# Kernel optimization log

Measured on AMD Instinct MI355X. Metric: run time of the kernel, lower is better.

Reference implementation:

```python
import jax, jax.numpy as jnp
import numpy as np

B, P, K = 8, 1024, 20
N = B * P
EMB, OUT = 1024, 40
GRID = 5

def _window(W):
    # Hamming taper (window_type='hamming')
    n = jnp.arange(W, dtype=jnp.float32)
    return 0.54 - 0.46 * jnp.cos(2.0 * jnp.pi * n / (W - 1))

def _init_kan(key, din, dout, W, S, g):
    nw = (din - W) // S + 1
    coeffs = jax.random.normal(key, (2, dout, nw, W, g), jnp.float32) / (np.sqrt(nw * W) * np.sqrt(g))
    bias = jnp.zeros((dout,), jnp.float32)
    return coeffs, bias

def stft_kan(x, coeffs, bias, W, S):
    # x: (n, D) -> (n, dout). Slice D into overlapping windows of size W,
    # stride S, apply Hamming taper, build Fourier features cos(k*x), sin(k*x)
    # for k=1..g and contract with learned coefficients (STFT-Fourier-KAN).
    nw, g = coeffs.shape[2], coeffs.shape[4]
    idx = (np.arange(nw) * S)[:, None] + np.arange(W)[None, :]        # (nw, W)
    xw = x[:, idx] * _window(W)                                        # (n, nw, W)
    kfreq = jnp.arange(1, g + 1, dtype=x.dtype)
    arg = xw[..., None] * kfreq                                        # (n, nw, W, g)
    y = (jnp.einsum('nwig,owig->no', jnp.cos(arg), coeffs[0])
         + jnp.einsum('nwig,owig->no', jnp.sin(arg), coeffs[1]))
    return y + bias

def setup_inputs():
    key = jax.random.key(0)
    ks = jax.random.split(key, 5)
    pos = jax.random.normal(ks[0], (N, 3), jnp.float32)
    batch = (jnp.arange(N) // P).astype(jnp.int32)  # sorted, equal-size clouds
    c1, b1 = _init_kan(ks[1], 6, 64, 3, 3, GRID)
    c2, b2 = _init_kan(ks[2], 64, 128, 16, 8, GRID)
    c3, b3 = _init_kan(ks[3], 128, EMB, 32, 16, GRID)
    c4, b4 = _init_kan(ks[4], 2 * EMB, OUT, 256, 128, GRID)
    return {"pos": pos, "batch": batch, "c1": c1, "b1": b1, "c2": c2, "b2": b2,
            "c3": c3, "b3": b3, "c4": c4, "b4": b4}

def reference(pos, batch, c1, b1, c2, b2, c3, b3, c4, b4):
    posb = pos.reshape(B, P, 3)
    # dynamic kNN graph per cloud (self excluded)
    d = jnp.sum((posb[:, :, None, :] - posb[:, None, :, :]) ** 2, -1)  # (B,P,P)
    d = d + jnp.eye(P, dtype=d.dtype) * 1e10
    _, nbr = jax.lax.top_k(-d, K)                                      # (B,P,K)
    pj = jax.vmap(lambda p, i: p[i])(posb, nbr)                        # (B,P,K,3)
    pi = jnp.broadcast_to(posb[:, :, None, :], pj.shape)
    e = jnp.concatenate([pi, pj - pi], -1).reshape(N * K, 6)           # edge feats
    h = stft_kan(e, c1, b1, 3, 3)                                      # (N*K,64)
    h = stft_kan(h, c2, b2, 16, 8)                                     # (N*K,128)
    x1 = jnp.max(h.reshape(N, K, 128), axis=1)                         # max aggr over neighbors
    x = stft_kan(x1, c3, b3, 32, 16)                                   # (N,EMB)
    gmax = jax.ops.segment_max(x, batch, num_segments=B)
    gsum = jax.ops.segment_sum(x, batch, num_segments=B)
    cnt = jax.ops.segment_sum(jnp.ones((N, 1), x.dtype), batch, num_segments=B)
    xg = jnp.concatenate([gmax, gsum / cnt], -1)                       # (B, 2*EMB)
    return stft_kan(xg, c4, b4, 256, 128)                              # (B, OUT)
```

## Files before the change

### kernel.cpp

```cpp
#include <hip/hip_runtime.h>


typedef unsigned short u16;
typedef unsigned int   u32;
typedef unsigned long long u64;
typedef __attribute__((ext_vector_type(8))) _Float16 half8;
typedef __attribute__((ext_vector_type(4))) float f32x4;

__device__ __forceinline__ float bf2f(u16 u) {
  u32 v = ((u32)u) << 16;
  return __uint_as_float(v);
}
__device__ __forceinline__ u16 f2bfr(float f) {
  u32 x = __float_as_uint(f);
  u32 r = x + 0x7FFFu + ((x >> 16) & 1u);
  return (u16)(r >> 16);
}
__device__ __forceinline__ u16 f2h(float f) {
  _Float16 h = (_Float16)f;
  u16 r;
  __builtin_memcpy(&r, &h, 2);
  return r;
}
__device__ __forceinline__ float h2f(u16 u) {
  _Float16 h;
  __builtin_memcpy(&h, &u, 2);
  return (float)h;
}
__device__ __forceinline__ float ldf(const void* p, size_t i, bool f32) {
  return f32 ? ((const float*)p)[i] : bf2f(((const u16*)p)[i]);
}
__device__ __forceinline__ u64 minu64(u64 a, u64 b) { return a < b ? a : b; }

__device__ __forceinline__ bool wave_detect(const void* pos) {
  float a = fabsf(((const float*)pos)[threadIdx.x & 63]);
  bool ok = (a > 1.0e-3f && a < 100.0f);
  unsigned long long m = __ballot(ok);
  return __popcll(m) >= 32;
}

#define NBR_OFF   ((size_t)0)
#define L4P_OFF   (((size_t)(1u << 20)) + 131072)
#define C1T_OFF   (((size_t)(1u << 20)) + 524288)
#define C2T_OFF   (((size_t)(1u << 20)) + 589824)
#define C3T_OFF   ((size_t)(2u << 20))
#define C4T_OFF   ((size_t)(7u << 20))
#define PMAX_OFF  ((size_t)(13u << 20))
#define PSUM_OFF  ((size_t)(14u << 20))
#define X1_OFF    ((size_t)(15u << 20))
#define H1_OFF    ((size_t)(18u << 20))

template <int DOUT, int NW, int WW, int KPAD, int OUTF32>
__device__ __forceinline__ void tkan_body(const void* __restrict__ src,
                                          void* __restrict__ dst,
                                          int id, bool f32) {
  constexpr int NA = NW * WW;
  constexpr int Kt = NA * 10;
  constexpr int OS = NA * 5;
  const int o = id / KPAD, f = id % KPAD;
  float v = 0.f;
  if (f < Kt) {
    const int part = f & 1, p = f >> 1;
    int aa, gg;
    if (p < 4 * NA) { aa = p >> 2;      gg = p & 3; }
    else            { aa = p - 4 * NA;  gg = 4;     }
    const int i = aa % WW, w = aa / WW;
    size_t sidx = (size_t)part * (DOUT * OS) + (size_t)o * OS +
                  (size_t)w * (WW * 5) + i * 5 + gg;
    v = ldf(src, sidx, f32);
  }
  if (OUTF32) ((float*)dst)[id] = v;
  else        ((u16*)dst)[id] = f2h(v);
}

__global__ __launch_bounds__(256) void prep_kernel(
    const void* __restrict__ pos, int* __restrict__ nbr,
    const void* __restrict__ s1, void* __restrict__ d1,
    const void* __restrict__ s2, void* __restrict__ d2,
    const void* __restrict__ s3, void* __restrict__ d3,
    const void* __restrict__ s4, void* __restrict__ d4) {
  __shared__ float px[1024], py[1024], pz[1024];
  const bool f32 = wave_detect(pos);
  const int blk = blockIdx.x;
  const int t = threadIdx.x;

  if (blk >= 2048) {
    const int tb = blk - 2048;
    if (tb < 16) {
      tkan_body<64, 2, 3, 64, 0>(s1, d1, tb * 256 + t, f32);
    } else if (tb < 576) {
      tkan_body<128, 7, 16, 1120, 0>(s2, d2, (tb - 16) * 256 + t, f32);
    } else if (tb < 9536) {
      tkan_body<1024, 7, 32, 2240, 0>(s3, d3, (tb - 576) * 256 + t, f32);
    } else {
      tkan_body<40, 15, 256, 38400, 1>(s4, d4, (tb - 9536) * 256 + t, f32);
    }
    return;
  }

  const int b = blk >> 8;
  const int x = blk & 255;
  const int base = b << 10;
  for (int j = t; j < 1024; j += 256) {
    size_t pidx = (size_t)(base + j) * 3;
    px[j] = ldf(pos, pidx, f32);
    py[j] = ldf(pos, pidx + 1, f32);
    pz[j] = ldf(pos, pidx + 2, f32);
  }
  __syncthreads();
  const int wv = t >> 6, lane = t & 63;
  const int q = x * 4 + wv;
  const float qx = px[q], qy = py[q], qz = pz[q];
  u64 key[16];
#pragma unroll
  for (int s = 0; s < 16; ++s) {
    const int j = s * 64 + lane;
    float dx = qx - px[j], dy = qy - py[j], dz = qz - pz[j];
    float d = __fadd_rn(__fadd_rn(__fmul_rn(dx, dx), __fmul_rn(dy, dy)),
                        __fmul_rn(dz, dz));
    key[s] = (j == q) ? ~0ull
                      : ((((u64)__float_as_uint(d)) << 32) | (u32)j);
  }
  const int obase = (base + q) * 20;
  for (int k = 0; k < 20; ++k) {
    u64 m = key[0];
#pragma unroll
    for (int s = 1; s < 16; ++s) m = minu64(m, key[s]);
#pragma unroll
    for (int off = 32; off >= 1; off >>= 1) {
      u32 lo = (u32)m, hi = (u32)(m >> 32);
      lo = __shfl_xor(lo, off, 64);
      hi = __shfl_xor(hi, off, 64);
      m = minu64(m, (((u64)hi) << 32) | lo);
    }
    if (lane == 0) nbr[obase + k] = (int)(u32)m;
#pragma unroll
    for (int s = 0; s < 16; ++s)
      if (key[s] == m) key[s] = ~0ull;
  }
}

template <int L>
__global__ __launch_bounds__(256, (L == 2) ? 2 : 3) void kan_kernel(
    const void* __restrict__ in_, const int* __restrict__ nbr,
    const void* __restrict__ pos, const u16* __restrict__ ct,
    const void* __restrict__ bias, void* __restrict__ out_,
    float* __restrict__ pmax, float* __restrict__ psum) {
  constexpr int W    = (L == 1) ? 3  : (L == 2) ? 16  : 32;
  constexpr int S    = (L == 1) ? 3  : (L == 2) ? 8   : 16;
  constexpr int DIN  = (L == 1) ? 6  : (L == 2) ? 64  : 128;
  constexpr int NT   = (L == 2) ? 128 : 64;
  constexpr int NW   = (DIN - W) / S + 1;
  constexpr int NA   = NW * W;
  constexpr int NPAIR = NA * 5;
  constexpr int S1P  = NA * 4;
  constexpr int KROW  = (L == 1) ? 64 : NPAIR * 2;
  constexpr int NCH   = KROW / 32;
  constexpr int NB    = NT / 16;
  constexpr int RW    = (L == 1) ? 64 : (L == 2) ? 80 : 32;
  constexpr int MB    = RW / 16;
  constexpr int PSTH  = DIN + 4;
  constexpr int LGW   = (W == 16) ? 4 : 5;
  constexpr int BCS   = NT * 8 + 8;
  constexpr int BBS   = 4 * BCS;
  constexpr int NPC   = NT / 64;

  __shared__ float hamS[(L == 1) ? 1 : W];
  __shared__ float wT1[(L == 1) ? 32 : 1];
  __shared__ int   hT1[(L == 1) ? 32 : 1];
  __shared__ u16   slab[(L == 1) ? 2 : 4 * RW * PSTH];
  __shared__ u16   stage1[(L == 1) ? 4 * 64 * 64 : 2];
  __shared__ u16   Bbuf[2 * BBS];

  const bool f32 = wave_detect(pos);
  const u16* inH = (const u16*)in_;
  const int t = threadIdx.x;
  if constexpr (L == 1) {
    if (t < 32) {
      float wv_ = 0.f; int hx = 0;
      if (t < NPAIR) {
        int aa, gg;
        if (t < S1P) { aa = t >> 2;   gg = t & 3; }
        else         { aa = t - S1P;  gg = 4;     }
        int i = aa % W;
        float hm = 0.54f - 0.46f * cospif(2.0f * (float)i / (float)(W - 1));
        wv_ = hm * (float)(gg + 1);
        hx = aa;
      }
      wT1[t] = wv_; hT1[t] = hx;
    }
  } else {
    if (t < W) hamS[t] = 0.54f - 0.46f * cospif(2.0f * (float)t / (float)(W - 1));
  }

  int tile, ncol0;
  if constexpr (L == 3) {
    const int id = blockIdx.x;
    tile = (id >> 3) & 63;
    ncol0 = ((((id & 7) << 1) | (id >> 9))) * NT;
  } else {
    tile = blockIdx.x;
    ncol0 = blockIdx.y * NT;
  }
  const int lane = t & 63, wv = t >> 6;
  const int m16 = lane & 15, kb = lane >> 4;
  const int rowbase = tile * (4 * RW) + wv * RW;
  u16* myslab = &slab[(L == 1) ? 0 : wv * RW * PSTH];

  const u16* srcB[NPC];
  int sdst[NPC];
#pragma unroll
  for (int p_ = 0; p_ < NPC; ++p_) {
    const int pid = t + p_ * 256;
    const int scol = pid >> 2, spart = pid & 3;
    srcB[p_] = ct + (size_t)(ncol0 + scol) * KROW + spart * 8;
    sdst[p_] = spart * BCS + scol * 8;
  }

  if constexpr (L >= 2) {
    constexpr int F4R = DIN / 4;
    constexpr int TOT = RW * F4R;
    for (int i = lane; i < TOT; i += 64) {
      const int r = i / F4R, c4 = i % F4R;
      *(uint2*)(myslab + r * PSTH + c4 * 4) =
          *(const uint2*)(inH + (size_t)(rowbase + r) * DIN + c4 * 4);
    }
  }

#pragma unroll
  for (int p_ = 0; p_ < NPC; ++p_) {
    const uint4 v = *(const uint4*)srcB[p_];
    *(uint4*)(Bbuf + sdst[p_]) = v;
  }
  __syncthreads();

  f32x4 acc[MB][NB];
#pragma unroll
  for (int mb = 0; mb < MB; ++mb)
#pragma unroll
    for (int nb = 0; nb < NB; ++nb) {
      acc[mb][nb][0] = 0.f; acc[mb][nb][1] = 0.f;
      acc[mb][nb][2] = 0.f; acc[mb][nb][3] = 0.f;
    }

  auto build_af = [&](int c, half8* af) {
    const int pg0 = c * 16 + kb * 4;
    if constexpr (L == 1) {
      float wm[4]; int hx[4]; bool val[4];
#pragma unroll
      for (int u = 0; u < 4; ++u) {
        const int pg = pg0 + u;
        wm[u] = wT1[pg]; hx[u] = hT1[pg]; val[u] = (pg < NPAIR);
      }
#pragma unroll
      for (int mb = 0; mb < MB; ++mb) {
        const int row = rowbase + mb * 16 + m16;
        const int pt = row / 20;
        const int cloud = pt >> 10, ci = pt & 1023;
        const int cb = cloud << 10;
        const int jl = nbr[row];
#pragma unroll
        for (int u = 0; u < 4; ++u) {
          float cs = 0.f, sn = 0.f;
          if (val[u]) {
            const int aa = hx[u];
            float v;
            if (aa < 3) {
              v = ldf(pos, (size_t)(cb + ci) * 3 + aa, f32);
            } else {
              const int cc2 = aa - 3;
              v = ldf(pos, (size_t)(cb + jl) * 3 + cc2, f32) -
                  ldf(pos, (size_t)(cb + ci) * 3 + cc2, f32);
            }
            const float ang = v * wm[u];
            cs = __cosf(ang); sn = __sinf(ang);
          }
          af[mb][2 * u]     = (_Float16)cs;
          af[mb][2 * u + 1] = (_Float16)sn;
        }
      }
    } else if (pg0 < S1P) {
      const int aa = pg0 >> 2;
      const int i = aa & (W - 1), w = aa >> LGW;
      const int hidx = S * w + i;
      const float hm = hamS[i];
#pragma unroll
      for (int mb = 0; mb < MB; ++mb) {
        const u16* rp = myslab + (mb * 16 + m16) * PSTH;
        const float th = h2f(rp[hidx]) * hm;
        const float c1 = __cosf(th), s1 = __sinf(th);
        const float tc = 2.0f * c1;
        const float c2 = tc * c1 - 1.0f, s2 = tc * s1;
        const float c3 = tc * c2 - c1,   s3 = tc * s2 - s1;
        const float c4 = tc * c3 - c2,   s4 = tc * s3 - s2;
        af[mb][0] = (_Float16)c1; af[mb][1] = (_Float16)s1;
        af[mb][2] = (_Float16)c2; af[mb][3] = (_Float16)s2;
        af[mb][4] = (_Float16)c3; af[mb][5] = (_Float16)s3;
        af[mb][6] = (_Float16)c4; af[mb][7] = (_Float16)s4;
      }
    } else {
      const int q0 = pg0 - S1P;
      float wm[4]; int hx[4];
#pragma unroll
      for (int u = 0; u < 4; ++u) {
        const int aa = q0 + u;
        const int i = aa & (W - 1), w = aa >> LGW;
        hx[u] = S * w + i;
        wm[u] = hamS[i] * 5.0f;
      }
#pragma unroll
      for (int mb = 0; mb < MB; ++mb) {
        const u16* rp = myslab + (mb * 16 + m16) * PSTH;
#pragma unroll
        for (int u = 0; u < 4; ++u) {
          const float ang = h2f(rp[hx[u]]) * wm[u];
          af[mb][2 * u]     = (_Float16)__cosf(ang);
          af[mb][2 * u + 1] = (_Float16)__sinf(ang);
        }
      }
    }
  };

  auto step = [&](int c, half8* afc, half8* afn) {
    const bool havenext = (c + 1 < NCH);
    uint4 bnext[NPC];
    if (havenext) {
#pragma unroll
      for (int p_ = 0; p_ < NPC; ++p_)
        bnext[p_] = *(const uint4*)(srcB[p_] + (c + 1) * 32);
    }
    if (havenext) build_af(c + 1, afn);
    const u16* bb = Bbuf + (c & 1) * BBS + kb * BCS;
#pragma unroll
    for (int nb = 0; nb < NB; ++nb) {
      const half8 bv = *(const half8*)(bb + (nb * 16 + m16) * 8);
#pragma unroll
      for (int mb = 0; mb < MB; ++mb)
        acc[mb][nb] = __builtin_amdgcn_mfma_f32_16x16x32_f16(
            afc[mb], bv, acc[mb][nb], 0, 0, 0);
    }
    if (havenext) {
#pragma unroll
      for (int p_ = 0; p_ < NPC; ++p_)
        *(uint4*)(Bbuf + ((c + 1) & 1) * BBS + sdst[p_]) = bnext[p_];
      __syncthreads();
    }
  };

  half8 afA[MB], afB[MB];
  build_af(0, afA);
  constexpr int NCH2 = (NCH / 2) * 2;
  for (int c = 0; c < NCH2; c += 2) {
    step(c, afA, afB);
    step(c + 1, afB, afA);
  }
  if constexpr ((NCH & 1) != 0) {
    step(NCH - 1, afA, afB);
  }

  if constexpr (L == 1) {
    u16* st = &stage1[wv * 4096];
#pragma unroll
    for (int mb = 0; mb < MB; ++mb)
#pragma unroll
      for (int nb = 0; nb < NB; ++nb) {
        const float bsv = ldf(bias, nb * 16 + m16, f32);
#pragma unroll
        for (int r = 0; r < 4; ++r)
          st[(mb * 16 + kb * 4 + r) * 64 + nb * 16 + m16] =
              f2h(acc[mb][nb][r] + bsv);
      }
    u16* gp = (u16*)out_ + (size_t)rowbase * 64;
    for (int i = lane; i < 512; i += 64)
      *(uint4*)(gp + i * 8) = *(const uint4*)&st[i * 8];
  } else if constexpr (L == 2) {
    u16* st = myslab;
    const int pbase = tile * 16 + wv * 4;
#pragma unroll
    for (int h = 0; h < 2; ++h) {
#pragma unroll
      for (int mb = 0; mb < MB; ++mb)
#pragma unroll
        for (int nb4 = 0; nb4 < 4; ++nb4) {
          const int nb = h * 4 + nb4;
          const float bsv = ldf(bias, ncol0 + nb * 16 + m16, f32);
#pragma unroll
          for (int r = 0; r < 4; ++r)
            st[(mb * 16 + kb * 4 + r) * PSTH + nb4 * 16 + m16] =
                f2h(acc[mb][nb][r] + bsv);
        }
#pragma unroll
      for (int j = 0; j < 4; ++j) {
        float m = -3.0e38f;
#pragma unroll
        for (int k = 0; k < 20; ++k)
          m = fmaxf(m, h2f(st[(j * 20 + k) * PSTH + lane]));
        ((u16*)out_)[(size_t)(pbase + j) * 128 + ncol0 + h * 64 + lane] = f2h(m);
      }
    }
  } else {
    const int chunk = rowbase >> 5;
#pragma unroll
    for (int nb = 0; nb < NB; ++nb) {
      const int col = ncol0 + nb * 16 + m16;
      const float bsv = ldf(bias, col, f32);
      float m = -3.0e38f, s = 0.f;
#pragma unroll
      for (int mb = 0; mb < MB; ++mb)
#pragma unroll
        for (int r = 0; r < 4; ++r) {
          const float v = acc[mb][nb][r] + bsv;
          m = fmaxf(m, v); s += v;
        }
#pragma unroll
      for (int off = 16; off <= 32; off <<= 1) {
        m = fmaxf(m, __shfl_xor(m, off, 64));
        s += __shfl_xor(s, off, 64);
      }
      if (kb == 0) {
        pmax[(size_t)chunk * 1024 + col] = m;
        psum[(size_t)chunk * 1024 + col] = s;
      }
    }
  }
}

__global__ __launch_bounds__(256) void l4_kernel(const float* __restrict__ pmax,
                                                 const float* __restrict__ psum,
                                                 const float* __restrict__ c4t,
                                                 float* __restrict__ part) {
  __shared__ float F[2560];
  const int t = threadIdx.x;
  const int w = blockIdx.x, b = blockIdx.y, z = blockIdx.z;
  const int ch = w * 128 + t;
  float xv;
  if (ch < 1024) {
    float m = -3.0e38f;
    for (int rc = 0; rc < 32; ++rc)
      m = fmaxf(m, pmax[(size_t)(b * 32 + rc) * 1024 + ch]);
    xv = m;
  } else {
    const int cc = ch - 1024;
    float s = 0.f;
    for (int rc = 0; rc < 32; ++rc)
      s += psum[(size_t)(b * 32 + rc) * 1024 + cc];
    xv = s * (1.0f / 1024.0f);
  }
  const float hm = 0.54f - 0.46f * cospif(2.0f * (float)t / 255.0f);
  const float aa = xv * hm;
  const float c1 = __cosf(aa), s1 = __sinf(aa);
  const float tc = 2.0f * c1;
  const float c2 = tc * c1 - 1.0f, s2 = tc * s1;
  const float c3 = tc * c2 - c1,   s3 = tc * s2 - s1;
  const float c4 = tc * c3 - c2,   s4 = tc * s3 - s2;
  const float a5 = aa * 5.0f;
  F[t * 8]     = c1; F[t * 8 + 1] = s1;
  F[t * 8 + 2] = c2; F[t * 8 + 3] = s2;
  F[t * 8 + 4] = c3; F[t * 8 + 5] = s3;
  F[t * 8 + 6] = c4; F[t * 8 + 7] = s4;
  F[2048 + t * 2]     = __cosf(a5);
  F[2048 + t * 2 + 1] = __sinf(a5);
  __syncthreads();
  if (t < 120) {
    const int o = t % 40, sl = t / 40;
    const int s = z * 3 + sl;
    const int f0 = s * 432;
    const int f1 = (f0 + 432 < 2560) ? (f0 + 432) : 2560;
    const float* cp1 = c4t + (size_t)o * 38400 + w * 2048;
    const float* cp2 = c4t + (size_t)o * 38400 + 30720 + w * 512;
    float acc = 0.f;
    for (int f = f0; f < f1; f += 4) {
      const float* cpf = (f < 2048) ? (cp1 + f) : (cp2 + (f - 2048));
      const float4 cv = *(const float4*)cpf;
      const float4 fa = *(const float4*)&F[f];
      acc += fa.x * cv.x + fa.y * cv.y + fa.z * cv.z + fa.w * cv.w;
    }
    part[((b * 15 + w) * 6 + s) * 40 + o] = acc;
  }
}

__global__ void outred_kernel(const float* __restrict__ part,
                              const void* __restrict__ b4,
                              const void* __restrict__ pos,
                              void* __restrict__ outp) {
  int t = threadIdx.x;
  const bool f32 = wave_detect(pos);
  if (t >= 320) return;
  int b = t / 40, o = t % 40;
  float s = ldf(b4, o, f32);
  for (int w = 0; w < 15; ++w)
#pragma unroll
    for (int sl = 0; sl < 6; ++sl)
      s += part[((b * 15 + w) * 6 + sl) * 40 + o];
  if (f32) ((float*)outp)[t] = s;
  else     ((u16*)outp)[t] = f2bfr(s);
}

extern "C" void kernel_launch(void* const* d_in, const int* in_sizes, int n_in,
                              void* d_out, int out_size, void* d_ws,
                              size_t ws_size, hipStream_t stream) {
  (void)in_sizes; (void)n_in; (void)out_size; (void)ws_size;
  const void* pos = d_in[0];
  const void* c1 = d_in[2];
  const void* b1 = d_in[3];
  const void* c2 = d_in[4];
  const void* b2 = d_in[5];
  const void* c3 = d_in[6];
  const void* b3 = d_in[7];
  const void* c4 = d_in[8];
  const void* b4 = d_in[9];

  char* ws = (char*)d_ws;
  int* nbr   = (int*)(ws + NBR_OFF);
  float* l4p = (float*)(ws + L4P_OFF);
  u16* c1t   = (u16*)(ws + C1T_OFF);
  u16* c2t   = (u16*)(ws + C2T_OFF);
  u16* c3t   = (u16*)(ws + C3T_OFF);
  float* c4t = (float*)(ws + C4T_OFF);
  float* pmax = (float*)(ws + PMAX_OFF);
  float* psum = (float*)(ws + PSUM_OFF);
  u16* x1    = (u16*)(ws + X1_OFF);
  u16* h1    = (u16*)(ws + H1_OFF);

  prep_kernel<<<17584, 256, 0, stream>>>(pos, nbr, c1, c1t, c2, c2t,
                                         c3, c3t, c4, c4t);

  kan_kernel<1><<<640, 256, 0, stream>>>(nullptr, nbr, pos, c1t, b1, h1,
                                         nullptr, nullptr);
  kan_kernel<2><<<dim3(512), 256, 0, stream>>>(h1, nullptr, pos, c2t,
                                               b2, x1, nullptr, nullptr);
  kan_kernel<3><<<1024, 256, 0, stream>>>(x1, nullptr, pos, c3t,
                                          b3, nullptr, pmax, psum);

  l4_kernel<<<dim3(15, 8, 2), 256, 0, stream>>>(pmax, psum, c4t, l4p);
  outred_kernel<<<1, 320, 0, stream>>>(l4p, b4, pos, d_out);
}
```

Before: 284.9 us.

## Fuse first KAN layer into second-layer kernel, dropping h1 intermediate buffer

```diff
diff --git a/kernel.cpp b/kernel.cpp
--- a/kernel.cpp
+++ b/kernel.cpp
@@ -48,7 +48,6 @@
 #define PMAX_OFF  ((size_t)(13u << 20))
 #define PSUM_OFF  ((size_t)(14u << 20))
 #define X1_OFF    ((size_t)(15u << 20))
-#define H1_OFF    ((size_t)(18u << 20))
 
 template <int DOUT, int NW, int WW, int KPAD, int OUTF32>
 __device__ __forceinline__ void tkan_body(const void* __restrict__ src,
@@ -145,19 +144,20 @@
     const void* __restrict__ in_, const int* __restrict__ nbr,
     const void* __restrict__ pos, const u16* __restrict__ ct,
     const void* __restrict__ bias, void* __restrict__ out_,
-    float* __restrict__ pmax, float* __restrict__ psum) {
-  constexpr int W    = (L == 1) ? 3  : (L == 2) ? 16  : 32;
-  constexpr int S    = (L == 1) ? 3  : (L == 2) ? 8   : 16;
-  constexpr int DIN  = (L == 1) ? 6  : (L == 2) ? 64  : 128;
+    float* __restrict__ pmax, float* __restrict__ psum,
+    const u16* __restrict__ ct1, const void* __restrict__ bias1) {
+  constexpr int W    = (L == 2) ? 16  : 32;
+  constexpr int S    = (L == 2) ? 8   : 16;
+  constexpr int DIN  = (L == 2) ? 64  : 128;
   constexpr int NT   = (L == 2) ? 128 : 64;
   constexpr int NW   = (DIN - W) / S + 1;
   constexpr int NA   = NW * W;
   constexpr int NPAIR = NA * 5;
   constexpr int S1P  = NA * 4;
-  constexpr int KROW  = (L == 1) ? 64 : NPAIR * 2;
+  constexpr int KROW  = NPAIR * 2;
   constexpr int NCH   = KROW / 32;
   constexpr int NB    = NT / 16;
-  constexpr int RW    = (L == 1) ? 64 : (L == 2) ? 80 : 32;
+  constexpr int RW    = (L == 2) ? 80 : 32;
   constexpr int MB    = RW / 16;
   constexpr int PSTH  = DIN + 4;
   constexpr int LGW   = (W == 16) ? 4 : 5;
@@ -165,32 +165,30 @@
   constexpr int BBS   = 4 * BCS;
   constexpr int NPC   = NT / 64;
 
-  __shared__ float hamS[(L == 1) ? 1 : W];
-  __shared__ float wT1[(L == 1) ? 32 : 1];
-  __shared__ int   hT1[(L == 1) ? 32 : 1];
-  __shared__ u16   slab[(L == 1) ? 2 : 4 * RW * PSTH];
-  __shared__ u16   stage1[(L == 1) ? 4 * 64 * 64 : 2];
+  __shared__ float hamS[W];
+  __shared__ float wT1[(L == 2) ? 32 : 1];
+  __shared__ int   hT1[(L == 2) ? 32 : 1];
+  __shared__ u16   slab[4 * RW * PSTH];
   __shared__ u16   Bbuf[2 * BBS];
 
   const bool f32 = wave_detect(pos);
   const u16* inH = (const u16*)in_;
   const int t = threadIdx.x;
-  if constexpr (L == 1) {
+  if (t < W) hamS[t] = 0.54f - 0.46f * cospif(2.0f * (float)t / (float)(W - 1));
+  if constexpr (L == 2) {
     if (t < 32) {
       float wv_ = 0.f; int hx = 0;
-      if (t < NPAIR) {
+      if (t < 30) {
         int aa, gg;
-        if (t < S1P) { aa = t >> 2;   gg = t & 3; }
-        else         { aa = t - S1P;  gg = 4;     }
-        int i = aa % W;
-        float hm = 0.54f - 0.46f * cospif(2.0f * (float)i / (float)(W - 1));
+        if (t < 24) { aa = t >> 2;  gg = t & 3; }
+        else        { aa = t - 24;  gg = 4;     }
+        int i = aa % 3;
+        float hm = 0.54f - 0.46f * cospif((float)i);
         wv_ = hm * (float)(gg + 1);
         hx = aa;
       }
       wT1[t] = wv_; hT1[t] = hx;
     }
-  } else {
-    if (t < W) hamS[t] = 0.54f - 0.46f * cospif(2.0f * (float)t / (float)(W - 1));
   }
 
   int tile, ncol0;
@@ -200,12 +198,12 @@
     ncol0 = ((((id & 7) << 1) | (id >> 9))) * NT;
   } else {
     tile = blockIdx.x;
-    ncol0 = blockIdx.y * NT;
+    ncol0 = 0;
   }
   const int lane = t & 63, wv = t >> 6;
   const int m16 = lane & 15, kb = lane >> 4;
   const int rowbase = tile * (4 * RW) + wv * RW;
-  u16* myslab = &slab[(L == 1) ? 0 : wv * RW * PSTH];
+  u16* myslab = &slab[wv * RW * PSTH];
 
   const u16* srcB[NPC];
   int sdst[NPC];
@@ -217,7 +215,7 @@
     sdst[p_] = spart * BCS + scol * 8;
   }
 
-  if constexpr (L >= 2) {
+  if constexpr (L == 3) {
     constexpr int F4R = DIN / 4;
     constexpr int TOT = RW * F4R;
     for (int i = lane; i < TOT; i += 64) {
@@ -234,26 +232,27 @@
   }
   __syncthreads();
 
-  f32x4 acc[MB][NB];
-#pragma unroll
-  for (int mb = 0; mb < MB; ++mb)
-#pragma unroll
-    for (int nb = 0; nb < NB; ++nb) {
-      acc[mb][nb][0] = 0.f; acc[mb][nb][1] = 0.f;
-      acc[mb][nb][2] = 0.f; acc[mb][nb][3] = 0.f;
-    }
-
-  auto build_af = [&](int c, half8* af) {
-    const int pg0 = c * 16 + kb * 4;
-    if constexpr (L == 1) {
+  if constexpr (L == 2) {
+    f32x4 acc1[5][4];
+#pragma unroll
+    for (int mb = 0; mb < 5; ++mb)
+#pragma unroll
+      for (int nb = 0; nb < 4; ++nb) {
+        acc1[mb][nb][0] = 0.f; acc1[mb][nb][1] = 0.f;
+        acc1[mb][nb][2] = 0.f; acc1[mb][nb][3] = 0.f;
+      }
+#pragma unroll
+    for (int c = 0; c < 2; ++c) {
+      const int pg0 = c * 16 + kb * 4;
       float wm[4]; int hx[4]; bool val[4];
 #pragma unroll
       for (int u = 0; u < 4; ++u) {
         const int pg = pg0 + u;
-        wm[u] = wT1[pg]; hx[u] = hT1[pg]; val[u] = (pg < NPAIR);
-      }
-#pragma unroll
-      for (int mb = 0; mb < MB; ++mb) {
+        wm[u] = wT1[pg]; hx[u] = hT1[pg]; val[u] = (pg < 30);
+      }
+      half8 af1[5];
+#pragma unroll
+      for (int mb = 0; mb < 5; ++mb) {
         const int row = rowbase + mb * 16 + m16;
         const int pt = row / 20;
         const int cloud = pt >> 10, ci = pt & 1023;
@@ -275,11 +274,44 @@
             const float ang = v * wm[u];
             cs = __cosf(ang); sn = __sinf(ang);
           }
-          af[mb][2 * u]     = (_Float16)cs;
-          af[mb][2 * u + 1] = (_Float16)sn;
+          af1[mb][2 * u]     = (_Float16)cs;
+          af1[mb][2 * u + 1] = (_Float16)sn;
         }
       }
-    } else if (pg0 < S1P) {
+#pragma unroll
+      for (int nb = 0; nb < 4; ++nb) {
+        const half8 bv = *(const half8*)(ct1 + (nb * 16 + m16) * 64 +
+                                         c * 32 + kb * 8);
+#pragma unroll
+        for (int mb = 0; mb < 5; ++mb)
+          acc1[mb][nb] = __builtin_amdgcn_mfma_f32_16x16x32_f16(
+              af1[mb], bv, acc1[mb][nb], 0, 0, 0);
+      }
+    }
+#pragma unroll
+    for (int mb = 0; mb < 5; ++mb)
+#pragma unroll
+      for (int nb = 0; nb < 4; ++nb) {
+        const float bsv = ldf(bias1, nb * 16 + m16, f32);
+#pragma unroll
+        for (int r = 0; r < 4; ++r)
+          myslab[(mb * 16 + kb * 4 + r) * PSTH + nb * 16 + m16] =
+              f2h(acc1[mb][nb][r] + bsv);
+      }
+  }
+
+  f32x4 acc[MB][NB];
+#pragma unroll
+  for (int mb = 0; mb < MB; ++mb)
+#pragma unroll
+    for (int nb = 0; nb < NB; ++nb) {
+      acc[mb][nb][0] = 0.f; acc[mb][nb][1] = 0.f;
+      acc[mb][nb][2] = 0.f; acc[mb][nb][3] = 0.f;
+    }
+
+  auto build_af = [&](int c, half8* af) {
+    const int pg0 = c * 16 + kb * 4;
+    if (pg0 < S1P) {
       const int aa = pg0 >> 2;
       const int i = aa & (W - 1), w = aa >> LGW;
       const int hidx = S * w + i;
@@ -358,22 +390,7 @@
     step(NCH - 1, afA, afB);
   }
 
-  if constexpr (L == 1) {
-    u16* st = &stage1[wv * 4096];
-#pragma unroll
-    for (int mb = 0; mb < MB; ++mb)
-#pragma unroll
-      for (int nb = 0; nb < NB; ++nb) {
-        const float bsv = ldf(bias, nb * 16 + m16, f32);
-#pragma unroll
-        for (int r = 0; r < 4; ++r)
-          st[(mb * 16 + kb * 4 + r) * 64 + nb * 16 + m16] =
-              f2h(acc[mb][nb][r] + bsv);
-      }
-    u16* gp = (u16*)out_ + (size_t)rowbase * 64;
-    for (int i = lane; i < 512; i += 64)
-      *(uint4*)(gp + i * 8) = *(const uint4*)&st[i * 8];
-  } else if constexpr (L == 2) {
+  if constexpr (L == 2) {
     u16* st = myslab;
     const int pbase = tile * 16 + wv * 4;
 #pragma unroll
@@ -383,7 +400,7 @@
 #pragma unroll
         for (int nb4 = 0; nb4 < 4; ++nb4) {
           const int nb = h * 4 + nb4;
-          const float bsv = ldf(bias, ncol0 + nb * 16 + m16, f32);
+          const float bsv = ldf(bias, nb * 16 + m16, f32);
 #pragma unroll
           for (int r = 0; r < 4; ++r)
             st[(mb * 16 + kb * 4 + r) * PSTH + nb4 * 16 + m16] =
@@ -395,7 +412,7 @@
 #pragma unroll
         for (int k = 0; k < 20; ++k)
           m = fmaxf(m, h2f(st[(j * 20 + k) * PSTH + lane]));
-        ((u16*)out_)[(size_t)(pbase + j) * 128 + ncol0 + h * 64 + lane] = f2h(m);
+        ((u16*)out_)[(size_t)(pbase + j) * 128 + h * 64 + lane] = f2h(m);
       }
     }
   } else {
@@ -520,17 +537,16 @@
   float* pmax = (float*)(ws + PMAX_OFF);
   float* psum = (float*)(ws + PSUM_OFF);
   u16* x1    = (u16*)(ws + X1_OFF);
-  u16* h1    = (u16*)(ws + H1_OFF);
 
   prep_kernel<<<17584, 256, 0, stream>>>(pos, nbr, c1, c1t, c2, c2t,
                                          c3, c3t, c4, c4t);
 
-  kan_kernel<1><<<640, 256, 0, stream>>>(nullptr, nbr, pos, c1t, b1, h1,
-                                         nullptr, nullptr);
-  kan_kernel<2><<<dim3(512), 256, 0, stream>>>(h1, nullptr, pos, c2t,
-                                               b2, x1, nullptr, nullptr);
+  kan_kernel<2><<<dim3(512), 256, 0, stream>>>(nullptr, nbr, pos, c2t,
+                                               b2, x1, nullptr, nullptr,
+                                               c1t, b1);
   kan_kernel<3><<<1024, 256, 0, stream>>>(x1, nullptr, pos, c3t,
-                                          b3, nullptr, pmax, psum);
+                                          b3, nullptr, pmax, psum,
+                                          nullptr, nullptr);
 
   l4_kernel<<<dim3(15, 8, 2), 256, 0, stream>>>(pmax, psum, c4t, l4p);
   outred_kernel<<<1, 320, 0, stream>>>(l4p, b4, pos, d_out);
```

Measured after the change: 279.6 us (median of 2 runs). Within noise of the previous version (-1.9%).
